# Kernel optimization log

Measured on AMD Instinct MI355X. Metric: run time of the kernel, lower is better.

The kernel has to match this reference:

```python
import jax, jax.numpy as jnp
import numpy as np

N_NODES = 100000
N_EDGES = 1600000
IN_DIM = 128
HID = 128
OUT_DIM = 64
EPS = 1e-8


def setup_inputs() -> dict:
    key = jax.random.key(0)
    ks = jax.random.split(key, 10)
    x = jax.random.normal(ks[0], (N_NODES, IN_DIM), dtype=jnp.float32)
    edge_index = jax.random.randint(ks[1], (2, N_EDGES), 0, N_NODES, dtype=jnp.int64)
    edge_attr = jax.random.uniform(ks[2], (N_EDGES, 4), dtype=jnp.float32)
    s1 = 1.0 / np.sqrt(IN_DIM)
    s2 = 1.0 / np.sqrt(HID)
    sr = 1.0 / np.sqrt(2 * HID)
    W1 = jax.random.normal(ks[3], (HID, IN_DIM), dtype=jnp.float32) * s1
    b1 = jnp.zeros((HID,), dtype=jnp.float32)
    W2 = jax.random.normal(ks[4], (HID, HID), dtype=jnp.float32) * s2
    b2 = jnp.zeros((HID,), dtype=jnp.float32)
    Wr = jax.random.normal(ks[5], (OUT_DIM, 2 * HID), dtype=jnp.float32) * sr
    br = jnp.zeros((OUT_DIM,), dtype=jnp.float32)
    return {"x": x, "edge_index": edge_index, "edge_attr": edge_attr,
            "W1": W1, "b1": b1, "W2": W2, "b2": b2, "Wr": Wr, "br": br}


def _edge_weight_from_attr_auto(edge_attr):
    # mean over features, min-max normalize, invert, clamp >= 0
    m = edge_attr.mean(axis=-1)                      # [E]
    m_min, m_max = m.min(), m.max()
    m_norm = (m - m_min) / (m_max - m_min + EPS)
    w = jnp.where(m_max - m_min > EPS, 1.0 - m_norm, jnp.ones_like(m))
    return jnp.clip(w, 0.0)


def reference(x, edge_index, edge_attr, W1, b1, W2, b2, Wr, br):
    N = x.shape[0]
    row, col = edge_index[0], edge_index[1]          # source -> target
    ew = _edge_weight_from_attr_auto(edge_attr)      # [E]
    # GCN normalization with self-loops (self-loop weight = 1.0)
    deg = jax.ops.segment_sum(ew, col, num_segments=N) + 1.0   # [N]
    dis = jax.lax.rsqrt(deg)                         # deg >= 1
    norm = dis[row] * ew * dis[col]                  # [E]

    def gcn(h, W, b):
        hW = h @ W.T                                 # [N, d_out]
        agg = jax.ops.segment_sum(norm[:, None] * hW[row], col, num_segments=N)
        # self-loop contribution: dis[i] * 1.0 * dis[i] * hW[i]
        return agg + (dis * dis)[:, None] * hW + b

    # dropout in eval mode -> identity
    h1 = jax.nn.relu(gcn(x, W1, b1))                 # [N, HID]
    h2 = jax.nn.relu(gcn(h1, W2, b2))                # [N, HID]
    hcat = jnp.concatenate([h1, h2], axis=-1)        # [N, 2*HID] (JK concat)
    return hcat @ Wr.T + br                          # residue-level [N, OUT_DIM]
```

## Files before the change

### kernel.cpp

```cpp
#include <hip/hip_runtime.h>

#define NN 100000
#define NE 1600000
#define HID 128
#define ODIM 64
#define NBK 196
#define BSHIFT 9
#define BGRID 512
#define CHUNK 3125
#define BITER 13
#define BINCAP 12288
#define SMAX 4504
#define LMAX 568

typedef unsigned int u32;
typedef unsigned short u16;
typedef __bf16 bf16x8 __attribute__((ext_vector_type(8)));
typedef float f32x4 __attribute__((ext_vector_type(4)));
typedef float f32x2 __attribute__((ext_vector_type(2)));

__device__ __forceinline__ float bf_lo(u32 p){ return __uint_as_float(p << 16); }
__device__ __forceinline__ float bf_hi(u32 p){ return __uint_as_float(p & 0xffff0000u); }
__device__ __forceinline__ u16 f2bf(float f){
  u32 u = __float_as_uint(f);
  u += 0x7fffu + ((u >> 16) & 1u);
  return (u16)(u >> 16);
}
__device__ __forceinline__ bf16x8 ld8bf(const u16* p){ return *(const bf16x8*)p; }
__device__ __forceinline__ bf16x8 cvt8(const float* p){
  union { bf16x8 v; u16 s[8]; } r;
#pragma unroll
  for (int i = 0; i < 8; i++) r.s[i] = f2bf(p[i]);
  return r.v;
}

__global__ __launch_bounds__(256) void k_prep(
    const float* __restrict__ W1, const float* __restrict__ W2,
    const float* __restrict__ Wr, u16* __restrict__ W1b, u16* __restrict__ W2b,
    u16* __restrict__ Wrb, u32* __restrict__ bcur, u32* __restrict__ minmax){
  int i = blockIdx.x * 256 + threadIdx.x;
  const float* src; u16* dst; int off;
  if (i < 4096){ src = W1; dst = W1b; off = i; }
  else if (i < 8192){ src = W2; dst = W2b; off = i - 4096; }
  else { src = Wr; dst = Wrb; off = i - 8192; }
  float4 v = ((const float4*)src)[off];
  uint2 o;
  o.x = (u32)f2bf(v.x) | ((u32)f2bf(v.y) << 16);
  o.y = (u32)f2bf(v.z) | ((u32)f2bf(v.w) << 16);
  ((uint2*)dst)[off] = o;
  if (blockIdx.x == 0){
    if (threadIdx.x < NBK) bcur[threadIdx.x] = (u32)threadIdx.x * BINCAP;
    if (threadIdx.x == 0){ minmax[0] = 0x7f800000u; minmax[1] = 0u; }
  }
}

__global__ __launch_bounds__(256) void k_bin(
    const float* __restrict__ eattr, const int* __restrict__ erow,
    const int* __restrict__ ecol, u32* __restrict__ bcur,
    uint2* __restrict__ bin, u32* __restrict__ minmax){
  __shared__ u32 lcnt[NBK], lofs[NBK], gb[NBK];
  __shared__ u32 scn[256];
  __shared__ u16 lmap[LMAX];
  __shared__ uint2 stage[SMAX];
  __shared__ u32 Tt;
  __shared__ float smin[4], smax[4];
  int tid = threadIdx.x;
  for (int t = tid; t < NBK; t += 256) lcnt[t] = 0;
  uint2 sent; sent.x = 0xFFFFFFFFu; sent.y = 0u;
  for (int t = tid; t < SMAX; t += 256) stage[t] = sent;
  __syncthreads();
  int base = blockIdx.x * CHUNK;
  float lmin = __uint_as_float(0x7f800000u), lmax = 0.f;
  u32 pk[BITER]; float mv[BITER]; u32 sv[BITER];
#pragma unroll
  for (int it = 0; it < BITER; it++){
    int idx = it * 256 + tid;
    u32 p = 0xFFFFFFFFu; float m = 0.f; u32 s = 0;
    if (idx < CHUNK){
      int e = base + idx;
      float4 a = ((const float4*)eattr)[e];
      m = 0.25f * (a.x + a.y + a.z + a.w);
      lmin = fminf(lmin, m); lmax = fmaxf(lmax, m);
      int c = ecol[e];
      s = (u32)erow[e]; if (s >= NN) s = 0;
      if ((u32)c < NN){
        u32 b = (u32)c >> BSHIFT;
        u32 r = atomicAdd(&lcnt[b], 1u);
        p = (b << 21) | (((u32)c & 511u) << 12) | r;
      }
    }
    pk[it] = p; mv[it] = m; sv[it] = s;
  }
  __syncthreads();
  u32 na = 0;
  if (tid < NBK) na = (lcnt[tid] + 7u) & ~7u;
  scn[tid] = na; __syncthreads();
  for (int s = 1; s < 256; s <<= 1){
    u32 t = (tid >= s) ? scn[tid - s] : 0;
    __syncthreads();
    scn[tid] += t;
    __syncthreads();
  }
  u32 ex = scn[tid] - na;
  if (tid < NBK){
    lofs[tid] = ex;
    u32 g = 0x80000000u;
    if (na){
      g = atomicAdd(&bcur[tid], na);
      if (g + na > (u32)(tid + 1) * BINCAP) g = 0x80000000u;
    }
    gb[tid] = g;
    for (u32 l = ex >> 3; l < (ex + na) >> 3; l++) lmap[l] = (u16)tid;
  }
  if (tid == 255) Tt = scn[255];
  __syncthreads();
#pragma unroll
  for (int it = 0; it < BITER; it++){
    u32 p = pk[it];
    if (p == 0xFFFFFFFFu) continue;
    uint2 rec; rec.x = sv[it] | (((p >> 12) & 511u) << 17); rec.y = __float_as_uint(mv[it]);
    stage[lofs[p >> 21] + (p & 4095u)] = rec;
  }
  __syncthreads();
  u32 T = Tt;
  for (u32 i = tid; i < T; i += 256){
    u32 b = lmap[i >> 3];
    u32 g = gb[b];
    if (g != 0x80000000u) bin[g + (i - lofs[b])] = stage[i];
  }
  for (int off = 32; off; off >>= 1){
    lmin = fminf(lmin, __shfl_xor(lmin, off));
    lmax = fmaxf(lmax, __shfl_xor(lmax, off));
  }
  int wid = tid >> 6, lane = tid & 63;
  if (lane == 0){ smin[wid] = lmin; smax[wid] = lmax; }
  __syncthreads();
  if (tid == 0){
    float mn = fminf(fminf(smin[0], smin[1]), fminf(smin[2], smin[3]));
    float mx = fmaxf(fmaxf(smax[0], smax[1]), fmaxf(smax[2], smax[3]));
    atomicMin(&minmax[0], __float_as_uint(mn));
    atomicMax(&minmax[1], __float_as_uint(mx));
  }
}

__global__ __launch_bounds__(1024) void k_sort(
    const u32* __restrict__ bcur, const uint2* __restrict__ bin,
    const u32* __restrict__ minmax, u32* __restrict__ csr,
    int* __restrict__ row_start, int* __restrict__ counts, float* __restrict__ dis){
  int b = blockIdx.x;
  int bb = b * BINCAP, be = (int)bcur[b];
  float mn  = __uint_as_float(minmax[0]);
  float mx  = __uint_as_float(minmax[1]);
  float rng = mx - mn;
  bool flat = !(rng > 1e-8f);
  float inv = 1.f / (rng + 1e-8f);
  __shared__ u32 cnt[512], off[512], cur[512], degfx[512];
  int tid = threadIdx.x;
  if (tid < 512){ cnt[tid] = 0; degfx[tid] = 0; }
  __syncthreads();
  for (int i = bb + tid; i < be; i += 1024){
    uint2 r = bin[i];
    if (r.x == 0xFFFFFFFFu) continue;
    u32 d = (r.x >> 17) & 511u;
    float w = flat ? 1.f : fmaxf(1.f - (__uint_as_float(r.y) - mn) * inv, 0.f);
    atomicAdd(&cnt[d], 1u);
    atomicAdd(&degfx[d], (u32)(w * 1048576.f + 0.5f));
  }
  __syncthreads();
  u32 v = 0;
  if (tid < 512){ v = cnt[tid]; off[tid] = v; }
  __syncthreads();
  for (int s = 1; s < 512; s <<= 1){
    u32 t = 0;
    if (tid < 512 && tid >= s) t = off[tid - s];
    __syncthreads();
    if (tid < 512) off[tid] += t;
    __syncthreads();
  }
  if (tid < 512){
    u32 ex = off[tid] - v;
    cur[tid] = ex;
    int node = (b << BSHIFT) + tid;
    if (node < NN){
      row_start[node] = bb + (int)ex;
      counts[node] = (int)v;
      dis[node] = rsqrtf(1.f + (float)degfx[tid] * (1.f / 1048576.f));
    }
  }
  __syncthreads();
  for (int i = bb + tid; i < be; i += 1024){
    uint2 r = bin[i];
    if (r.x == 0xFFFFFFFFu) continue;
    u32 d = (r.x >> 17) & 511u;
    float w = flat ? 1.f : fmaxf(1.f - (__uint_as_float(r.y) - mn) * inv, 0.f);
    u32 wq = (u32)(w * 32767.f + 0.5f);
    u32 pos = (u32)bb + atomicAdd(&cur[d], 1u);
    csr[pos] = (r.x & 0x1FFFFu) | (wq << 17);
  }
}

template <bool A_F32>
__global__ __launch_bounds__(256) void k_gemm128(
    const void* __restrict__ Av, const u16* __restrict__ Bt,
    const float* __restrict__ dis, u16* __restrict__ G){
  int wave = threadIdx.x >> 6, lane = threadIdx.x & 63;
  int m0 = blockIdx.x * 16;
  int m = lane & 15, q = lane >> 4;
  const float* arow_f = (const float*)Av + (size_t)(m0 + m) * HID;
  const u16*   arow_b = (const u16*)Av   + (size_t)(m0 + m) * HID;
  const u16* brow0 = Bt + (size_t)(wave * 16 + m) * HID;
  const u16* brow1 = brow0 + (size_t)64 * HID;
  f32x4 acc0 = {0.f, 0.f, 0.f, 0.f}, acc1 = {0.f, 0.f, 0.f, 0.f};
#pragma unroll
  for (int kb = 0; kb < HID; kb += 32){
    bf16x8 af = A_F32 ? cvt8(arow_f + kb + q * 8) : ld8bf(arow_b + kb + q * 8);
    acc0 = __builtin_amdgcn_mfma_f32_16x16x32_bf16(af, ld8bf(brow0 + kb + q * 8), acc0, 0, 0, 0);
    acc1 = __builtin_amdgcn_mfma_f32_16x16x32_bf16(af, ld8bf(brow1 + kb + q * 8), acc1, 0, 0, 0);
  }
  u16* crow = G + (size_t)(m0 + q * 4) * HID + wave * 16 + m;
#pragma unroll
  for (int r = 0; r < 4; r++){
    float d = dis[m0 + q * 4 + r];
    crow[(size_t)r * HID]      = f2bf(acc0[r] * d);
    crow[(size_t)r * HID + 64] = f2bf(acc1[r] * d);
  }
}

__global__ __launch_bounds__(256) void k_aggregate(
    const int* __restrict__ row_start, const int* __restrict__ counts,
    const u32* __restrict__ csr, const float* __restrict__ dis,
    const u16* __restrict__ g, const float* __restrict__ bias,
    u16* __restrict__ hout){
  int node = blockIdx.x * 4 + (threadIdx.x >> 6);
  int lane = threadIdx.x & 63;
  int s = row_start[node], c = counts[node];
  const u32* gp = (const u32*)g;
  u32 sv = gp[((size_t)node << 6) + lane];
  f32x2 acc = {bf_lo(sv), bf_hi(sv)};
  for (int base = 0; base < c; base += 64){
    int nch = min(64, c - base);
    u32 sidx = 0; float ws = 0.f;
    if (lane < nch){
      u32 pw = csr[s + base + lane];
      sidx = pw & 0x1FFFFu;
      ws = (float)(pw >> 17) * (1.f / 32767.f);
    }
    u32 wsb = __float_as_uint(ws);
    int j = 0;
#define GATH(T) \
    for (; j + T <= nch; j += T){ \
      u32 pv[T]; float wv[T]; \
      _Pragma("unroll") \
      for (int t = 0; t < T; t++){ \
        u32 st = (u32)__builtin_amdgcn_readlane(sidx, j + t); \
        wv[t] = __uint_as_float(__builtin_amdgcn_readlane(wsb, j + t)); \
        const u32* rowp = gp + st * 64u;          \
        pv[t] = rowp[lane]; \
      } \
      _Pragma("unroll") \
      for (int t = 0; t < T; t++){ \
        f32x2 val = {bf_lo(pv[t]), bf_hi(pv[t])}; \
        acc += wv[t] * val; \
      } \
    }
    GATH(16)
    GATH(8)
    GATH(4)
#undef GATH
    for (; j < nch; ++j){
      u32 st = (u32)__builtin_amdgcn_readlane(sidx, j);
      float wt = __uint_as_float(__builtin_amdgcn_readlane(wsb, j));
      const u32* rowp = gp + st * 64u;
      u32 pv = rowp[lane];
      f32x2 val = {bf_lo(pv), bf_hi(pv)};
      acc += wt * val;
    }
  }
  float di = dis[node];
  float2 bv = ((const float2*)bias)[lane];
  float o0 = fmaxf(acc.x * di + bv.x, 0.f);
  float o1 = fmaxf(acc.y * di + bv.y, 0.f);
  ((u32*)hout)[((size_t)node << 6) + lane] = (u32)f2bf(o0) | ((u32)f2bf(o1) << 16);
}

__global__ __launch_bounds__(256) void k_readout(
    const u16* __restrict__ h1, const u16* __restrict__ h2,
    const u16* __restrict__ Wrb, const float* __restrict__ br, float* __restrict__ out){
  int wave = threadIdx.x >> 6, lane = threadIdx.x & 63;
  int m0 = blockIdx.x * 16;
  int n0 = wave * 16;
  int m = lane & 15, q = lane >> 4;
  const u16* a1 = h1 + (size_t)(m0 + m) * HID;
  const u16* a2 = h2 + (size_t)(m0 + m) * HID;
  const u16* b  = Wrb + (size_t)(n0 + m) * (2 * HID);
  f32x4 acc = {0.f, 0.f, 0.f, 0.f};
#pragma unroll
  for (int kb = 0; kb < HID; kb += 32){
    acc = __builtin_amdgcn_mfma_f32_16x16x32_bf16(
        ld8bf(a1 + kb + q * 8), ld8bf(b + kb + q * 8), acc, 0, 0, 0);
  }
#pragma unroll
  for (int kb = 0; kb < HID; kb += 32){
    acc = __builtin_amdgcn_mfma_f32_16x16x32_bf16(
        ld8bf(a2 + kb + q * 8), ld8bf(b + HID + kb + q * 8), acc, 0, 0, 0);
  }
  float bias = br[n0 + m];
  float* crow = out + (size_t)(m0 + q * 4) * ODIM + n0 + m;
#pragma unroll
  for (int r = 0; r < 4; r++) crow[(size_t)r * ODIM] = acc[r] + bias;
}

extern "C" void kernel_launch(void* const* d_in, const int* in_sizes, int n_in,
                              void* d_out, int out_size, void* d_ws, size_t ws_size,
                              hipStream_t stream){
  const float* x     = (const float*)d_in[0];
  const int*   eidx  = (const int*)d_in[1];
  const float* eattr = (const float*)d_in[2];
  const float* W1    = (const float*)d_in[3];
  const float* b1    = (const float*)d_in[4];
  const float* W2    = (const float*)d_in[5];
  const float* b2    = (const float*)d_in[6];
  const float* Wr    = (const float*)d_in[7];
  const float* br    = (const float*)d_in[8];
  const int* erow  = eidx;
  const int* ecol  = eidx + NE;

  char* w = (char*)d_ws;
  auto carve = [&](size_t bytes) -> void* {
    void* p = (void*)w;
    w += (bytes + 255) & ~(size_t)255;
    return p;
  };
  u32* csr       = (u32*)carve((size_t)NBK * BINCAP * 4);
  u32* bcur      = (u32*)carve(256 * 4);
  u32* minmax    = (u32*)carve(256);
  int* row_start = (int*)carve((size_t)NN * 4);
  int* counts    = (int*)carve((size_t)NN * 4);
  float* dis     = (float*)carve((size_t)NN * 4);
  u16* W1b       = (u16*)carve((size_t)HID * HID * 2);
  u16* W2b       = (u16*)carve((size_t)HID * HID * 2);
  u16* Wrb       = (u16*)carve((size_t)ODIM * 2 * HID * 2);
  u16* g         = (u16*)carve((size_t)NN * HID * 2);
  u16* h1        = (u16*)carve((size_t)NN * HID * 2);
  u16* h2        = (u16*)carve((size_t)NN * HID * 2);
  uint2* bin     = (uint2*)h2;

  k_prep<<<48, 256, 0, stream>>>(W1, W2, Wr, W1b, W2b, Wrb, bcur, minmax);
  k_bin<<<BGRID, 256, 0, stream>>>(eattr, erow, ecol, bcur, bin, minmax);
  k_sort<<<NBK, 1024, 0, stream>>>(bcur, bin, minmax, csr, row_start, counts, dis);

  k_gemm128<true><<<NN / 16, 256, 0, stream>>>(x, W1b, dis, g);
  k_aggregate<<<NN / 4, 256, 0, stream>>>(row_start, counts, csr, dis, g, b1, h1);
  k_gemm128<false><<<NN / 16, 256, 0, stream>>>(h1, W2b, dis, g);
  k_aggregate<<<NN / 4, 256, 0, stream>>>(row_start, counts, csr, dis, g, b2, h2);
  k_readout<<<NN / 16, 256, 0, stream>>>(h1, h2, Wrb, br, (float*)d_out);
}
```

Measured before the change: 418.2 us.

## Fuse weight prep into binning, tile GEMMs 32 rows, add nontemporal gathers

```diff
diff --git a/kernel.cpp b/kernel.cpp
--- a/kernel.cpp
+++ b/kernel.cpp
@@ -7,6 +7,7 @@
 #define NBK 196
 #define BSHIFT 9
 #define BGRID 512
+#define CVTB 48
 #define CHUNK 3125
 #define BITER 13
 #define BINCAP 12288
@@ -34,40 +35,34 @@
   return r.v;
 }
 
-__global__ __launch_bounds__(256) void k_prep(
-    const float* __restrict__ W1, const float* __restrict__ W2,
-    const float* __restrict__ Wr, u16* __restrict__ W1b, u16* __restrict__ W2b,
-    u16* __restrict__ Wrb, u32* __restrict__ bcur, u32* __restrict__ minmax){
-  int i = blockIdx.x * 256 + threadIdx.x;
-  const float* src; u16* dst; int off;
-  if (i < 4096){ src = W1; dst = W1b; off = i; }
-  else if (i < 8192){ src = W2; dst = W2b; off = i - 4096; }
-  else { src = Wr; dst = Wrb; off = i - 8192; }
-  float4 v = ((const float4*)src)[off];
-  uint2 o;
-  o.x = (u32)f2bf(v.x) | ((u32)f2bf(v.y) << 16);
-  o.y = (u32)f2bf(v.z) | ((u32)f2bf(v.w) << 16);
-  ((uint2*)dst)[off] = o;
-  if (blockIdx.x == 0){
-    if (threadIdx.x < NBK) bcur[threadIdx.x] = (u32)threadIdx.x * BINCAP;
-    if (threadIdx.x == 0){ minmax[0] = 0x7f800000u; minmax[1] = 0u; }
-  }
-}
-
 __global__ __launch_bounds__(256) void k_bin(
     const float* __restrict__ eattr, const int* __restrict__ erow,
     const int* __restrict__ ecol, u32* __restrict__ bcur,
-    uint2* __restrict__ bin, u32* __restrict__ minmax){
+    uint2* __restrict__ bin, u32* __restrict__ minmax,
+    const float* __restrict__ W1, const float* __restrict__ W2,
+    const float* __restrict__ Wr, u16* __restrict__ W1b,
+    u16* __restrict__ W2b, u16* __restrict__ Wrb){
+  int tid = threadIdx.x;
+  if (blockIdx.x >= BGRID){
+    int i = (blockIdx.x - BGRID) * 256 + tid;
+    const float* src; u16* dst; int off;
+    if (i < 4096){ src = W1; dst = W1b; off = i; }
+    else if (i < 8192){ src = W2; dst = W2b; off = i - 4096; }
+    else { src = Wr; dst = Wrb; off = i - 8192; }
+    float4 v = ((const float4*)src)[off];
+    uint2 o;
+    o.x = (u32)f2bf(v.x) | ((u32)f2bf(v.y) << 16);
+    o.y = (u32)f2bf(v.z) | ((u32)f2bf(v.w) << 16);
+    ((uint2*)dst)[off] = o;
+    return;
+  }
   __shared__ u32 lcnt[NBK], lofs[NBK], gb[NBK];
   __shared__ u32 scn[256];
   __shared__ u16 lmap[LMAX];
   __shared__ uint2 stage[SMAX];
   __shared__ u32 Tt;
   __shared__ float smin[4], smax[4];
-  int tid = threadIdx.x;
   for (int t = tid; t < NBK; t += 256) lcnt[t] = 0;
-  uint2 sent; sent.x = 0xFFFFFFFFu; sent.y = 0u;
-  for (int t = tid; t < SMAX; t += 256) stage[t] = sent;
   __syncthreads();
   int base = blockIdx.x * CHUNK;
   float lmin = __uint_as_float(0x7f800000u), lmax = 0.f;
@@ -92,8 +87,8 @@
     pk[it] = p; mv[it] = m; sv[it] = s;
   }
   __syncthreads();
-  u32 na = 0;
-  if (tid < NBK) na = (lcnt[tid] + 7u) & ~7u;
+  u32 na = 0, n = 0;
+  if (tid < NBK){ n = lcnt[tid]; na = (n + 7u) & ~7u; }
   scn[tid] = na; __syncthreads();
   for (int s = 1; s < 256; s <<= 1){
     u32 t = (tid >= s) ? scn[tid - s] : 0;
@@ -106,11 +101,13 @@
     lofs[tid] = ex;
     u32 g = 0x80000000u;
     if (na){
-      g = atomicAdd(&bcur[tid], na);
-      if (g + na > (u32)(tid + 1) * BINCAP) g = 0x80000000u;
+      u32 gl = atomicAdd(&bcur[tid], na);
+      if (gl + na <= BINCAP) g = (u32)tid * BINCAP + gl;
     }
     gb[tid] = g;
     for (u32 l = ex >> 3; l < (ex + na) >> 3; l++) lmap[l] = (u16)tid;
+    uint2 sent; sent.x = 0xFFFFFFFFu; sent.y = 0u;
+    for (u32 k = n; k < na; k++) stage[ex + k] = sent;
   }
   if (tid == 255) Tt = scn[255];
   __syncthreads();
@@ -138,7 +135,7 @@
   if (tid == 0){
     float mn = fminf(fminf(smin[0], smin[1]), fminf(smin[2], smin[3]));
     float mx = fmaxf(fmaxf(smax[0], smax[1]), fmaxf(smax[2], smax[3]));
-    atomicMin(&minmax[0], __float_as_uint(mn));
+    atomicMax(&minmax[0], ~__float_as_uint(mn));
     atomicMax(&minmax[1], __float_as_uint(mx));
   }
 }
@@ -148,8 +145,8 @@
     const u32* __restrict__ minmax, u32* __restrict__ csr,
     int* __restrict__ row_start, int* __restrict__ counts, float* __restrict__ dis){
   int b = blockIdx.x;
-  int bb = b * BINCAP, be = (int)bcur[b];
-  float mn  = __uint_as_float(minmax[0]);
+  int bb = b * BINCAP, be = bb + (int)bcur[b];
+  float mn  = __uint_as_float(~minmax[0]);
   float mx  = __uint_as_float(minmax[1]);
   float rng = mx - mn;
   bool flat = !(rng > 1e-8f);
@@ -204,25 +201,37 @@
     const void* __restrict__ Av, const u16* __restrict__ Bt,
     const float* __restrict__ dis, u16* __restrict__ G){
   int wave = threadIdx.x >> 6, lane = threadIdx.x & 63;
-  int m0 = blockIdx.x * 16;
+  int m0 = blockIdx.x * 32;
   int m = lane & 15, q = lane >> 4;
-  const float* arow_f = (const float*)Av + (size_t)(m0 + m) * HID;
-  const u16*   arow_b = (const u16*)Av   + (size_t)(m0 + m) * HID;
+  const float* a0f = (const float*)Av + (size_t)(m0 + m) * HID;
+  const float* a1f = a0f + (size_t)16 * HID;
+  const u16*   a0b = (const u16*)Av   + (size_t)(m0 + m) * HID;
+  const u16*   a1b = a0b + (size_t)16 * HID;
   const u16* brow0 = Bt + (size_t)(wave * 16 + m) * HID;
   const u16* brow1 = brow0 + (size_t)64 * HID;
-  f32x4 acc0 = {0.f, 0.f, 0.f, 0.f}, acc1 = {0.f, 0.f, 0.f, 0.f};
+  f32x4 acc00 = {0.f,0.f,0.f,0.f}, acc01 = {0.f,0.f,0.f,0.f};
+  f32x4 acc10 = {0.f,0.f,0.f,0.f}, acc11 = {0.f,0.f,0.f,0.f};
 #pragma unroll
   for (int kb = 0; kb < HID; kb += 32){
-    bf16x8 af = A_F32 ? cvt8(arow_f + kb + q * 8) : ld8bf(arow_b + kb + q * 8);
-    acc0 = __builtin_amdgcn_mfma_f32_16x16x32_bf16(af, ld8bf(brow0 + kb + q * 8), acc0, 0, 0, 0);
-    acc1 = __builtin_amdgcn_mfma_f32_16x16x32_bf16(af, ld8bf(brow1 + kb + q * 8), acc1, 0, 0, 0);
-  }
-  u16* crow = G + (size_t)(m0 + q * 4) * HID + wave * 16 + m;
+    bf16x8 af0 = A_F32 ? cvt8(a0f + kb + q * 8) : ld8bf(a0b + kb + q * 8);
+    bf16x8 af1 = A_F32 ? cvt8(a1f + kb + q * 8) : ld8bf(a1b + kb + q * 8);
+    bf16x8 bf0 = ld8bf(brow0 + kb + q * 8);
+    bf16x8 bf1 = ld8bf(brow1 + kb + q * 8);
+    acc00 = __builtin_amdgcn_mfma_f32_16x16x32_bf16(af0, bf0, acc00, 0, 0, 0);
+    acc01 = __builtin_amdgcn_mfma_f32_16x16x32_bf16(af0, bf1, acc01, 0, 0, 0);
+    acc10 = __builtin_amdgcn_mfma_f32_16x16x32_bf16(af1, bf0, acc10, 0, 0, 0);
+    acc11 = __builtin_amdgcn_mfma_f32_16x16x32_bf16(af1, bf1, acc11, 0, 0, 0);
+  }
+  u16* crow0 = G + (size_t)(m0 + q * 4) * HID + wave * 16 + m;
+  u16* crow1 = crow0 + (size_t)16 * HID;
 #pragma unroll
   for (int r = 0; r < 4; r++){
-    float d = dis[m0 + q * 4 + r];
-    crow[(size_t)r * HID]      = f2bf(acc0[r] * d);
-    crow[(size_t)r * HID + 64] = f2bf(acc1[r] * d);
+    float d0 = dis[m0 + q * 4 + r];
+    float d1 = dis[m0 + 16 + q * 4 + r];
+    crow0[(size_t)r * HID]      = f2bf(acc00[r] * d0);
+    crow0[(size_t)r * HID + 64] = f2bf(acc01[r] * d0);
+    crow1[(size_t)r * HID]      = f2bf(acc10[r] * d1);
+    crow1[(size_t)r * HID + 64] = f2bf(acc11[r] * d1);
   }
 }
 
@@ -241,7 +250,7 @@
     int nch = min(64, c - base);
     u32 sidx = 0; float ws = 0.f;
     if (lane < nch){
-      u32 pw = csr[s + base + lane];
+      u32 pw = __builtin_nontemporal_load(&csr[s + base + lane]);
       sidx = pw & 0x1FFFFu;
       ws = (float)(pw >> 17) * (1.f / 32767.f);
     }
@@ -255,7 +264,7 @@
         u32 st = (u32)__builtin_amdgcn_readlane(sidx, j + t); \
         wv[t] = __uint_as_float(__builtin_amdgcn_readlane(wsb, j + t)); \
         const u32* rowp = gp + st * 64u;          \
-        pv[t] = rowp[lane]; \
+        pv[t] = __builtin_nontemporal_load(rowp + lane); \
       } \
       _Pragma("unroll") \
       for (int t = 0; t < T; t++){ \
@@ -271,7 +280,7 @@
       u32 st = (u32)__builtin_amdgcn_readlane(sidx, j);
       float wt = __uint_as_float(__builtin_amdgcn_readlane(wsb, j));
       const u32* rowp = gp + st * 64u;
-      u32 pv = rowp[lane];
+      u32 pv = __builtin_nontemporal_load(rowp + lane);
       f32x2 val = {bf_lo(pv), bf_hi(pv)};
       acc += wt * val;
     }
@@ -287,27 +296,35 @@
     const u16* __restrict__ h1, const u16* __restrict__ h2,
     const u16* __restrict__ Wrb, const float* __restrict__ br, float* __restrict__ out){
   int wave = threadIdx.x >> 6, lane = threadIdx.x & 63;
-  int m0 = blockIdx.x * 16;
+  int m0 = blockIdx.x * 32;
   int n0 = wave * 16;
   int m = lane & 15, q = lane >> 4;
-  const u16* a1 = h1 + (size_t)(m0 + m) * HID;
-  const u16* a2 = h2 + (size_t)(m0 + m) * HID;
+  const u16* a10 = h1 + (size_t)(m0 + m) * HID;
+  const u16* a11 = a10 + (size_t)16 * HID;
+  const u16* a20 = h2 + (size_t)(m0 + m) * HID;
+  const u16* a21 = a20 + (size_t)16 * HID;
   const u16* b  = Wrb + (size_t)(n0 + m) * (2 * HID);
-  f32x4 acc = {0.f, 0.f, 0.f, 0.f};
+  f32x4 acc0 = {0.f,0.f,0.f,0.f}, acc1 = {0.f,0.f,0.f,0.f};
 #pragma unroll
   for (int kb = 0; kb < HID; kb += 32){
-    acc = __builtin_amdgcn_mfma_f32_16x16x32_bf16(
-        ld8bf(a1 + kb + q * 8), ld8bf(b + kb + q * 8), acc, 0, 0, 0);
+    bf16x8 bf = ld8bf(b + kb + q * 8);
+    acc0 = __builtin_amdgcn_mfma_f32_16x16x32_bf16(ld8bf(a10 + kb + q * 8), bf, acc0, 0, 0, 0);
+    acc1 = __builtin_amdgcn_mfma_f32_16x16x32_bf16(ld8bf(a11 + kb + q * 8), bf, acc1, 0, 0, 0);
   }
 #pragma unroll
   for (int kb = 0; kb < HID; kb += 32){
-    acc = __builtin_amdgcn_mfma_f32_16x16x32_bf16(
-        ld8bf(a2 + kb + q * 8), ld8bf(b + HID + kb + q * 8), acc, 0, 0, 0);
+    bf16x8 bf = ld8bf(b + HID + kb + q * 8);
+    acc0 = __builtin_amdgcn_mfma_f32_16x16x32_bf16(ld8bf(a20 + kb + q * 8), bf, acc0, 0, 0, 0);
+    acc1 = __builtin_amdgcn_mfma_f32_16x16x32_bf16(ld8bf(a21 + kb + q * 8), bf, acc1, 0, 0, 0);
   }
   float bias = br[n0 + m];
-  float* crow = out + (size_t)(m0 + q * 4) * ODIM + n0 + m;
-#pragma unroll
-  for (int r = 0; r < 4; r++) crow[(size_t)r * ODIM] = acc[r] + bias;
+  float* crow0 = out + (size_t)(m0 + q * 4) * ODIM + n0 + m;
+  float* crow1 = crow0 + (size_t)16 * ODIM;
+#pragma unroll
+  for (int r = 0; r < 4; r++){
+    crow0[(size_t)r * ODIM] = acc0[r] + bias;
+    crow1[(size_t)r * ODIM] = acc1[r] + bias;
+  }
 }
 
 extern "C" void kernel_launch(void* const* d_in, const int* in_sizes, int n_in,
@@ -345,13 +362,14 @@
   u16* h2        = (u16*)carve((size_t)NN * HID * 2);
   uint2* bin     = (uint2*)h2;
 
-  k_prep<<<48, 256, 0, stream>>>(W1, W2, Wr, W1b, W2b, Wrb, bcur, minmax);
-  k_bin<<<BGRID, 256, 0, stream>>>(eattr, erow, ecol, bcur, bin, minmax);
+  hipMemsetAsync(bcur, 0, 1024 + 256, stream);
+  k_bin<<<BGRID + CVTB, 256, 0, stream>>>(eattr, erow, ecol, bcur, bin, minmax,
+                                          W1, W2, Wr, W1b, W2b, Wrb);
   k_sort<<<NBK, 1024, 0, stream>>>(bcur, bin, minmax, csr, row_start, counts, dis);
 
-  k_gemm128<true><<<NN / 16, 256, 0, stream>>>(x, W1b, dis, g);
+  k_gemm128<true><<<NN / 32, 256, 0, stream>>>(x, W1b, dis, g);
   k_aggregate<<<NN / 4, 256, 0, stream>>>(row_start, counts, csr, dis, g, b1, h1);
-  k_gemm128<false><<<NN / 16, 256, 0, stream>>>(h1, W2b, dis, g);
+  k_gemm128<false><<<NN / 32, 256, 0, stream>>>(h1, W2b, dis, g);
   k_aggregate<<<NN / 4, 256, 0, stream>>>(row_start, counts, csr, dis, g, b2, h2);
-  k_readout<<<NN / 16, 256, 0, stream>>>(h1, h2, Wrb, br, (float*)d_out);
-}
+  k_readout<<<NN / 32, 256, 0, stream>>>(h1, h2, Wrb, br, (float*)d_out);
+}
```

Result: slower. 443.0 us (+5.9%).
